# Performance work log

Hardware: AMD Instinct MI355X
Metric: run time of the kernel (lower is better)

Reference implementation:

```python
import jax, jax.numpy as jnp
import numpy as np


def squash(x, axis=-1):
    # norm_sq/(1+norm_sq) * x/norm, exactly as the torch version
    norm_sq = jnp.sum(x * x, axis=axis, keepdims=True)
    norm = jnp.sqrt(norm_sq)
    return norm_sq / (1.0 + norm_sq) * (x / norm)


def setup_inputs() -> dict:
    key = jax.random.key(0)
    k1, k2 = jax.random.split(key)
    batch, in_caps, in_hid, out_caps, out_hid = 128, 1152, 16, 32, 16
    input_capsules = jax.random.normal(k1, (batch, in_caps, in_hid), dtype=jnp.float32)
    # EinMix weight: 'in_caps in_hid out_caps out_hid'
    W = jax.random.normal(k2, (in_caps, in_hid, out_caps, out_hid), dtype=jnp.float32) * 0.05
    return {"input_capsules": input_capsules, "W": W, "routing_iterations": 3}


def reference(input_capsules, W, routing_iterations):
    # U: [batch, in_caps, out_caps, out_hid]
    U = jnp.einsum('bih,ihoj->bioj', input_capsules, W)
    batch, in_caps, out_caps, out_hid = U.shape
    B = jnp.zeros((batch, in_caps, out_caps), dtype=U.dtype)
    V = None
    for _ in range(routing_iterations):
        C = jax.nn.softmax(B, axis=-1)           # [b, i, o]
        S = jnp.einsum('bio,bioh->boh', C, U)    # [b, o, h]
        V = squash(S, axis=-1)                   # [b, o, h]
        B = B + jnp.einsum('bioh,boh->bio', U, V)
    return V
```

## Files before the change

### kernel.cpp

```cpp
#include <hip/hip_runtime.h>
#include <hip/hip_bf16.h>


#define IN_CAPS 1152
#define OUT_CAPS 32
#define BATCH 128
#define IPC 18
#define NBLK_I (IN_CAPS / IPC)
#define SV_ELEMS (BATCH * OUT_CAPS * 16)

typedef __attribute__((ext_vector_type(8))) short short8;
typedef __attribute__((ext_vector_type(4))) float f32x4;

__device__ inline unsigned f2bf(float x) {
  unsigned u = __builtin_bit_cast(unsigned, x);
  return (u + 0x7FFFu + ((u >> 16) & 1u)) >> 16;
}

__global__ __launch_bounds__(256) void conv_w(const float* __restrict__ W,
                                              unsigned short* __restrict__ Wb) {
  __shared__ float st[16 * 516];
  const int t = threadIdx.x;
  const size_t ibase = (size_t)blockIdx.x * 8192;
  const float4* src = (const float4*)(W + ibase);
#pragma unroll
  for (int r = 0; r < 8; ++r) {
    const int f = r * 256 + t;
    const int k = f >> 7, c4 = f & 127;
    *(float4*)&st[k * 516 + c4 * 4] = src[f];
  }
  __syncthreads();
  unsigned short* dst = Wb + ibase;
#pragma unroll
  for (int r = 0; r < 4; ++r) {
    const int u = r * 256 + t;
    const int o = u >> 5, l = u & 31;
    const int col = o * 16 + (l & 15), k0 = (l >> 4) * 8;
    unsigned b[8];
#pragma unroll
    for (int j = 0; j < 8; ++j) b[j] = f2bf(st[(k0 + j) * 516 + col]);
    uint4 outv;
    outv.x = b[0] | (b[1] << 16);
    outv.y = b[2] | (b[3] << 16);
    outv.z = b[4] | (b[5] << 16);
    outv.w = b[6] | (b[7] << 16);
    *(uint4*)(dst + (size_t)u * 8) = outv;
  }
}

__device__ __forceinline__ void build_xs(const float* __restrict__ X, int bg,
                                         int i0, int t, unsigned (*xs)[64][4]) {
#pragma unroll
  for (int rep = 0; rep < IPC * 256 / 512; ++rep) {
    const int base = rep * 512 + t;
    const int ii = base >> 8;
    const int e = base & 255;
    const int l2 = e >> 2, ju = e & 3;
    unsigned val = 0;
    if (l2 < 32) {
      const float2 f = *(const float2*)(X +
          ((size_t)(bg * 16 + (l2 & 15)) * IN_CAPS + (i0 + ii)) * 16 +
          (l2 >> 4) * 8 + 2 * ju);
      val = f2bf(f.x) | (f2bf(f.y) << 16);
    }
    xs[ii][l2][ju] = val;
  }
}

__device__ __forceinline__ short8 ld_x(const unsigned (*xs)[64][4], int ii, int l) {
  return __builtin_bit_cast(short8, *(const uint4*)(&xs[ii][l][0]));
}

__global__ __launch_bounds__(512, 4)
void caps_pass1(const unsigned short* __restrict__ Wb,
                const float* __restrict__ X, float* __restrict__ P) {
  __shared__ __align__(16) unsigned xs[IPC][64][4];
  const int t = threadIdx.x, w = t >> 6, l = t & 63;
  const int q = l >> 4, bl = l & 15;
  const int gx = blockIdx.x, iblk = gx & 63, bg = gx >> 6;
  const int i0 = iblk * IPC;

  build_xs(X, bg, i0, t, xs);
  __syncthreads();

  const short8* wp = (const short8*)Wb + ((size_t)i0 * 32 + w * 4) * 32 + (l & 31);
  f32x4 sacc[4];
#pragma unroll
  for (int m = 0; m < 4; ++m) sacc[m] = (f32x4){0.f, 0.f, 0.f, 0.f};

  for (int ii = 0; ii < IPC; ++ii) {
    short8 x = ld_x(xs, ii, l);
    short8 a0 = wp[0], a1 = wp[32], a2 = wp[64], a3 = wp[96];
    wp += 1024;
    sacc[0] = __builtin_amdgcn_mfma_f32_16x16x32_bf16(a0, x, sacc[0], 0, 0, 0);
    sacc[1] = __builtin_amdgcn_mfma_f32_16x16x32_bf16(a1, x, sacc[1], 0, 0, 0);
    sacc[2] = __builtin_amdgcn_mfma_f32_16x16x32_bf16(a2, x, sacc[2], 0, 0, 0);
    sacc[3] = __builtin_amdgcn_mfma_f32_16x16x32_bf16(a3, x, sacc[3], 0, 0, 0);
  }
  float* pp = P + ((size_t)iblk * 128 + bg * 16 + bl) * 512 + w * 64 + q * 4;
#pragma unroll
  for (int m = 0; m < 4; ++m) *(f32x4*)(pp + m * 16) = sacc[m] * (1.f / 32.f);
}

__global__ __launch_bounds__(512, 4)
void caps_pass23(const unsigned short* __restrict__ Wb,
                 const float* __restrict__ X,
                 const float* __restrict__ Vt,
                 float* __restrict__ P) {
  __shared__ __align__(16) unsigned xs[IPC][64][4];
  __shared__ float part[2][8][16];
  const int t = threadIdx.x, w = t >> 6, l = t & 63;
  const int q = l >> 4, bl = l & 15;
  const int gx = blockIdx.x, iblk = gx & 63, bg = gx >> 6;
  const int i0 = iblk * IPC;

  f32x4 v[4], sacc[4];
#pragma unroll
  for (int m = 0; m < 4; ++m) {
    v[m] = ((const f32x4*)Vt)[((size_t)(bg * 8 + w) * 64 + l) * 4 + m];
    sacc[m] = (f32x4){0.f, 0.f, 0.f, 0.f};
  }

  build_xs(X, bg, i0, t, xs);
  __syncthreads();

  const short8* wp = (const short8*)Wb + ((size_t)i0 * 32 + w * 4) * 32 + (l & 31);
  short8 an[4];
  short8 xn = ld_x(xs, 0, l);
#pragma unroll
  for (int m = 0; m < 4; ++m) an[m] = wp[m * 32];
  wp += 1024;

  for (int ii = 0; ii < IPC; ++ii) {
    short8 ac[4];
#pragma unroll
    for (int m = 0; m < 4; ++m) ac[m] = an[m];
    short8 xc = xn;
    if (ii + 1 < IPC) {
      xn = ld_x(xs, ii + 1, l);
#pragma unroll
      for (int m = 0; m < 4; ++m) an[m] = wp[m * 32];
      wp += 1024;
    }

    const f32x4 z = {0.f, 0.f, 0.f, 0.f};
    f32x4 d[4];
#pragma unroll
    for (int m = 0; m < 4; ++m)
      d[m] = __builtin_amdgcn_mfma_f32_16x16x32_bf16(ac[m], xc, z, 0, 0, 0);

    float e[4];
#pragma unroll
    for (int m = 0; m < 4; ++m) {
      f32x4 pr = d[m] * v[m];
      float p = (pr[0] + pr[1]) + (pr[2] + pr[3]);
      p += __shfl_xor(p, 16);
      p += __shfl_xor(p, 32);
      e[m] = __expf(p);
    }
    const float esum = (e[0] + e[1]) + (e[2] + e[3]);
    if (q == 0) part[ii & 1][w][bl] = esum;
    __syncthreads();
    float den = 0.f;
#pragma unroll
    for (int ww = 0; ww < 8; ++ww) den += part[ii & 1][ww][bl];
    const float rden = __builtin_amdgcn_rcpf(den);
#pragma unroll
    for (int m = 0; m < 4; ++m) sacc[m] += d[m] * (e[m] * rden);
  }

  float* pp = P + ((size_t)iblk * 128 + bg * 16 + bl) * 512 + w * 64 + q * 4;
#pragma unroll
  for (int m = 0; m < 4; ++m) *(f32x4*)(pp + m * 16) = sacc[m];
}

template <int MODE>
__global__ __launch_bounds__(256)
void reduce_squash(const float* __restrict__ P, float* __restrict__ Vt,
                   float* __restrict__ V1p, float* __restrict__ Out) {
  const int j = blockIdx.x * 256 + threadIdx.x;
  float s = 0.f;
  const float* p = P + j;
#pragma unroll 8
  for (int k = 0; k < NBLK_I; ++k) s += p[(size_t)k * SV_ELEMS];
  float ns = s * s;
  ns += __shfl_xor(ns, 1);
  ns += __shfl_xor(ns, 2);
  ns += __shfl_xor(ns, 4);
  ns += __shfl_xor(ns, 8);
  const float sc = ns / ((1.f + ns) * sqrtf(ns));
  float vv = s * sc;
  if constexpr (MODE == 2) {
    Out[j] = vv;
  } else {
    if constexpr (MODE == 0) V1p[j] = vv;
    if constexpr (MODE == 1) vv += V1p[j];
    const int b = j >> 9, oh = j & 511, o = oh >> 4, h = oh & 15;
    const int bg = b >> 4, bl = b & 15, w = o >> 2, m = o & 3, qq = h >> 2;
    Vt[(((size_t)(bg * 8 + w) * 64 + qq * 16 + bl) * 16) + m * 4 + (h & 3)] = vv;
  }
}

extern "C" void kernel_launch(void* const* d_in, const int* in_sizes, int n_in,
                              void* d_out, int out_size, void* d_ws, size_t ws_size,
                              hipStream_t stream) {
  const float* X  = (const float*)d_in[0];
  const float* Wg = (const float*)d_in[1];

  float* P   = (float*)d_ws;
  float* Vt  = P + (size_t)NBLK_I * SV_ELEMS;
  float* V1p = Vt + SV_ELEMS;
  unsigned short* Wb = (unsigned short*)(V1p + SV_ELEMS);
  float* out = (float*)d_out;

  conv_w<<<IN_CAPS, 256, 0, stream>>>(Wg, Wb);

  caps_pass1<<<512, 512, 0, stream>>>(Wb, X, P);
  reduce_squash<0><<<256, 256, 0, stream>>>(P, Vt, V1p, nullptr);

  caps_pass23<<<512, 512, 0, stream>>>(Wb, X, Vt, P);
  reduce_squash<1><<<256, 256, 0, stream>>>(P, Vt, V1p, nullptr);

  caps_pass23<<<512, 512, 0, stream>>>(Wb, X, Vt, P);
  reduce_squash<2><<<256, 256, 0, stream>>>(P, nullptr, nullptr, out);
}
```

Measured before the change: 164.9 us.

## Fuse all capsule routing stages into one cooperative kernel with grid syncs

Replaces the seven separate launches (weight conversion, three routing passes, three reductions) with one cooperative kernel that separates phases using grid-wide syncs. Shared memory is reused between the weight transpose staging and the X tile. The aim is to remove per-launch overhead and inter-kernel gaps. The costs are grid barrier overhead and a reduction phase that now uses only a quarter of the threads, concentrated in the first blocks. The old multi-kernel path is kept as a fallback if the cooperative launch fails.

```diff
diff --git a/kernel.cpp b/kernel.cpp
--- a/kernel.cpp
+++ b/kernel.cpp
@@ -1,5 +1,8 @@
 #include <hip/hip_runtime.h>
 #include <hip/hip_bf16.h>
+#include <hip/hip_cooperative_groups.h>
+
+namespace cg = cooperative_groups;
 
 
 #define IN_CAPS 1152
@@ -8,6 +11,7 @@
 #define IPC 18
 #define NBLK_I (IN_CAPS / IPC)
 #define SV_ELEMS (BATCH * OUT_CAPS * 16)
+#define GRID 512
 
 typedef __attribute__((ext_vector_type(8))) short short8;
 typedef __attribute__((ext_vector_type(4))) float f32x4;
@@ -15,37 +19,6 @@
 __device__ inline unsigned f2bf(float x) {
   unsigned u = __builtin_bit_cast(unsigned, x);
   return (u + 0x7FFFu + ((u >> 16) & 1u)) >> 16;
-}
-
-__global__ __launch_bounds__(256) void conv_w(const float* __restrict__ W,
-                                              unsigned short* __restrict__ Wb) {
-  __shared__ float st[16 * 516];
-  const int t = threadIdx.x;
-  const size_t ibase = (size_t)blockIdx.x * 8192;
-  const float4* src = (const float4*)(W + ibase);
-#pragma unroll
-  for (int r = 0; r < 8; ++r) {
-    const int f = r * 256 + t;
-    const int k = f >> 7, c4 = f & 127;
-    *(float4*)&st[k * 516 + c4 * 4] = src[f];
-  }
-  __syncthreads();
-  unsigned short* dst = Wb + ibase;
-#pragma unroll
-  for (int r = 0; r < 4; ++r) {
-    const int u = r * 256 + t;
-    const int o = u >> 5, l = u & 31;
-    const int col = o * 16 + (l & 15), k0 = (l >> 4) * 8;
-    unsigned b[8];
-#pragma unroll
-    for (int j = 0; j < 8; ++j) b[j] = f2bf(st[(k0 + j) * 516 + col]);
-    uint4 outv;
-    outv.x = b[0] | (b[1] << 16);
-    outv.y = b[2] | (b[3] << 16);
-    outv.z = b[4] | (b[5] << 16);
-    outv.w = b[6] | (b[7] << 16);
-    *(uint4*)(dst + (size_t)u * 8) = outv;
-  }
 }
 
 __device__ __forceinline__ void build_xs(const float* __restrict__ X, int bg,
@@ -71,23 +44,43 @@
   return __builtin_bit_cast(short8, *(const uint4*)(&xs[ii][l][0]));
 }
 
-__global__ __launch_bounds__(512, 4)
-void caps_pass1(const unsigned short* __restrict__ Wb,
-                const float* __restrict__ X, float* __restrict__ P) {
-  __shared__ __align__(16) unsigned xs[IPC][64][4];
-  const int t = threadIdx.x, w = t >> 6, l = t & 63;
-  const int q = l >> 4, bl = l & 15;
-  const int gx = blockIdx.x, iblk = gx & 63, bg = gx >> 6;
-  const int i0 = iblk * IPC;
-
-  build_xs(X, bg, i0, t, xs);
-  __syncthreads();
-
-  const short8* wp = (const short8*)Wb + ((size_t)i0 * 32 + w * 4) * 32 + (l & 31);
+__device__ __forceinline__ void conv_i(const float* __restrict__ W,
+                                       unsigned short* __restrict__ Wb,
+                                       float* st, int i, int t) {
+  const float4* src = (const float4*)(W + (size_t)i * 8192);
+#pragma unroll
+  for (int r = 0; r < 4; ++r) {
+    const int f = r * 512 + t;
+    const int k = f >> 7, c4 = f & 127;
+    *(float4*)&st[k * 516 + c4 * 4] = src[f];
+  }
+  __syncthreads();
+  unsigned short* dst = Wb + (size_t)i * 8192;
+#pragma unroll
+  for (int r = 0; r < 2; ++r) {
+    const int uu = r * 512 + t;
+    const int o = uu >> 5, ll = uu & 31;
+    const int col = o * 16 + (ll & 15), k0 = (ll >> 4) * 8;
+    unsigned b[8];
+#pragma unroll
+    for (int j = 0; j < 8; ++j) b[j] = f2bf(st[(k0 + j) * 516 + col]);
+    uint4 outv;
+    outv.x = b[0] | (b[1] << 16);
+    outv.y = b[2] | (b[3] << 16);
+    outv.z = b[4] | (b[5] << 16);
+    outv.w = b[6] | (b[7] << 16);
+    *(uint4*)(dst + (size_t)uu * 8) = outv;
+  }
+  __syncthreads();
+}
+
+__device__ __forceinline__ void pass1_phase(const short8* __restrict__ wpb,
+                                            const unsigned (*xs)[64][4],
+                                            float* __restrict__ pp, int l) {
+  const short8* wp = wpb;
   f32x4 sacc[4];
 #pragma unroll
   for (int m = 0; m < 4; ++m) sacc[m] = (f32x4){0.f, 0.f, 0.f, 0.f};
-
   for (int ii = 0; ii < IPC; ++ii) {
     short8 x = ld_x(xs, ii, l);
     short8 a0 = wp[0], a1 = wp[32], a2 = wp[64], a3 = wp[96];
@@ -97,23 +90,16 @@
     sacc[2] = __builtin_amdgcn_mfma_f32_16x16x32_bf16(a2, x, sacc[2], 0, 0, 0);
     sacc[3] = __builtin_amdgcn_mfma_f32_16x16x32_bf16(a3, x, sacc[3], 0, 0, 0);
   }
-  float* pp = P + ((size_t)iblk * 128 + bg * 16 + bl) * 512 + w * 64 + q * 4;
 #pragma unroll
   for (int m = 0; m < 4; ++m) *(f32x4*)(pp + m * 16) = sacc[m] * (1.f / 32.f);
 }
 
-__global__ __launch_bounds__(512, 4)
-void caps_pass23(const unsigned short* __restrict__ Wb,
-                 const float* __restrict__ X,
-                 const float* __restrict__ Vt,
-                 float* __restrict__ P) {
-  __shared__ __align__(16) unsigned xs[IPC][64][4];
-  __shared__ float part[2][8][16];
-  const int t = threadIdx.x, w = t >> 6, l = t & 63;
-  const int q = l >> 4, bl = l & 15;
-  const int gx = blockIdx.x, iblk = gx & 63, bg = gx >> 6;
-  const int i0 = iblk * IPC;
-
+__device__ __forceinline__ void pass23_phase(const short8* __restrict__ wpb,
+                                             const unsigned (*xs)[64][4],
+                                             float (*part)[8][16],
+                                             const float* __restrict__ Vt,
+                                             float* __restrict__ pp,
+                                             int bg, int w, int l, int q, int bl) {
   f32x4 v[4], sacc[4];
 #pragma unroll
   for (int m = 0; m < 4; ++m) {
@@ -121,10 +107,7 @@
     sacc[m] = (f32x4){0.f, 0.f, 0.f, 0.f};
   }
 
-  build_xs(X, bg, i0, t, xs);
-  __syncthreads();
-
-  const short8* wp = (const short8*)Wb + ((size_t)i0 * 32 + w * 4) * 32 + (l & 31);
+  const short8* wp = wpb;
   short8 an[4];
   short8 xn = ld_x(xs, 0, l);
 #pragma unroll
@@ -169,9 +152,139 @@
     for (int m = 0; m < 4; ++m) sacc[m] += d[m] * (e[m] * rden);
   }
 
+#pragma unroll
+  for (int m = 0; m < 4; ++m) *(f32x4*)(pp + m * 16) = sacc[m];
+}
+
+template <int MODE>
+__device__ __forceinline__ void reduce_phase(const float* __restrict__ P,
+                                             float* __restrict__ Vt,
+                                             float* __restrict__ V1p,
+                                             float* __restrict__ Out, int j) {
+  if (j < SV_ELEMS) {
+    float s = 0.f;
+    const float* p = P + j;
+#pragma unroll 8
+    for (int k = 0; k < NBLK_I; ++k) s += p[(size_t)k * SV_ELEMS];
+    float ns = s * s;
+    ns += __shfl_xor(ns, 1);
+    ns += __shfl_xor(ns, 2);
+    ns += __shfl_xor(ns, 4);
+    ns += __shfl_xor(ns, 8);
+    const float sc = ns / ((1.f + ns) * sqrtf(ns));
+    float vv = s * sc;
+    if constexpr (MODE == 2) {
+      Out[j] = vv;
+    } else {
+      if constexpr (MODE == 0) V1p[j] = vv;
+      if constexpr (MODE == 1) vv += V1p[j];
+      const int b = j >> 9, oh = j & 511, o = oh >> 4, h = oh & 15;
+      const int bg = b >> 4, bl = b & 15, w = o >> 2, m = o & 3, qq = h >> 2;
+      Vt[(((size_t)(bg * 8 + w) * 64 + qq * 16 + bl) * 16) + m * 4 + (h & 3)] = vv;
+    }
+  }
+}
+
+__global__ __launch_bounds__(512, 4)
+void caps_fused(const float* __restrict__ W, const float* __restrict__ X,
+                unsigned short* __restrict__ Wb, float* __restrict__ P,
+                float* __restrict__ Vt, float* __restrict__ V1p,
+                float* __restrict__ Out) {
+  __shared__ __align__(16) char smem[16 * 516 * 4];
+  float* st = (float*)smem;
+  unsigned (*xs)[64][4] = (unsigned (*)[64][4])smem;
+  float (*part)[8][16] = (float (*)[8][16])(smem + IPC * 64 * 16);
+
+  const int t = threadIdx.x, w = t >> 6, l = t & 63;
+  const int q = l >> 4, bl = l & 15;
+  const int bid = blockIdx.x, iblk = bid & 63, bg = bid >> 6;
+  const int i0 = iblk * IPC;
+  const int gt = bid * 512 + t;
+  cg::grid_group grid = cg::this_grid();
+
+  for (int i = bid; i < IN_CAPS; i += GRID) conv_i(W, Wb, st, i, t);
+
+  build_xs(X, bg, i0, t, xs);
+  __syncthreads();
+  grid.sync();
+
+  const short8* wpb = (const short8*)Wb + ((size_t)i0 * 32 + w * 4) * 32 + (l & 31);
   float* pp = P + ((size_t)iblk * 128 + bg * 16 + bl) * 512 + w * 64 + q * 4;
-#pragma unroll
-  for (int m = 0; m < 4; ++m) *(f32x4*)(pp + m * 16) = sacc[m];
+
+  pass1_phase(wpb, xs, pp, l);
+  grid.sync();
+  reduce_phase<0>(P, Vt, V1p, nullptr, gt);
+  grid.sync();
+  pass23_phase(wpb, xs, part, Vt, pp, bg, w, l, q, bl);
+  grid.sync();
+  reduce_phase<1>(P, Vt, V1p, nullptr, gt);
+  grid.sync();
+  pass23_phase(wpb, xs, part, Vt, pp, bg, w, l, q, bl);
+  grid.sync();
+  reduce_phase<2>(P, nullptr, nullptr, Out, gt);
+}
+
+__global__ __launch_bounds__(256) void conv_w(const float* __restrict__ W,
+                                              unsigned short* __restrict__ Wb) {
+  __shared__ float st[16 * 516];
+  const int t = threadIdx.x;
+  const size_t ibase = (size_t)blockIdx.x * 8192;
+  const float4* src = (const float4*)(W + ibase);
+#pragma unroll
+  for (int r = 0; r < 8; ++r) {
+    const int f = r * 256 + t;
+    const int k = f >> 7, c4 = f & 127;
+    *(float4*)&st[k * 516 + c4 * 4] = src[f];
+  }
+  __syncthreads();
+  unsigned short* dst = Wb + ibase;
+#pragma unroll
+  for (int r = 0; r < 4; ++r) {
+    const int u = r * 256 + t;
+    const int o = u >> 5, l = u & 31;
+    const int col = o * 16 + (l & 15), k0 = (l >> 4) * 8;
+    unsigned b[8];
+#pragma unroll
+    for (int j = 0; j < 8; ++j) b[j] = f2bf(st[(k0 + j) * 516 + col]);
+    uint4 outv;
+    outv.x = b[0] | (b[1] << 16);
+    outv.y = b[2] | (b[3] << 16);
+    outv.z = b[4] | (b[5] << 16);
+    outv.w = b[6] | (b[7] << 16);
+    *(uint4*)(dst + (size_t)u * 8) = outv;
+  }
+}
+
+__global__ __launch_bounds__(512, 4)
+void caps_pass1(const unsigned short* __restrict__ Wb,
+                const float* __restrict__ X, float* __restrict__ P) {
+  __shared__ __align__(16) unsigned xs[IPC][64][4];
+  const int t = threadIdx.x, w = t >> 6, l = t & 63;
+  const int q = l >> 4, bl = l & 15;
+  const int gx = blockIdx.x, iblk = gx & 63, bg = gx >> 6;
+  const int i0 = iblk * IPC;
+  build_xs(X, bg, i0, t, xs);
+  __syncthreads();
+  const short8* wpb = (const short8*)Wb + ((size_t)i0 * 32 + w * 4) * 32 + (l & 31);
+  float* pp = P + ((size_t)iblk * 128 + bg * 16 + bl) * 512 + w * 64 + q * 4;
+  pass1_phase(wpb, xs, pp, l);
+}
+
+__global__ __launch_bounds__(512, 4)
+void caps_pass23(const unsigned short* __restrict__ Wb,
+                 const float* __restrict__ X,
+                 const float* __restrict__ Vt, float* __restrict__ P) {
+  __shared__ __align__(16) unsigned xs[IPC][64][4];
+  __shared__ float part[2][8][16];
+  const int t = threadIdx.x, w = t >> 6, l = t & 63;
+  const int q = l >> 4, bl = l & 15;
+  const int gx = blockIdx.x, iblk = gx & 63, bg = gx >> 6;
+  const int i0 = iblk * IPC;
+  build_xs(X, bg, i0, t, xs);
+  __syncthreads();
+  const short8* wpb = (const short8*)Wb + ((size_t)i0 * 32 + w * 4) * 32 + (l & 31);
+  float* pp = P + ((size_t)iblk * 128 + bg * 16 + bl) * 512 + w * 64 + q * 4;
+  pass23_phase(wpb, xs, part, Vt, pp, bg, w, l, q, bl);
 }
 
 template <int MODE>
@@ -179,26 +292,7 @@
 void reduce_squash(const float* __restrict__ P, float* __restrict__ Vt,
                    float* __restrict__ V1p, float* __restrict__ Out) {
   const int j = blockIdx.x * 256 + threadIdx.x;
-  float s = 0.f;
-  const float* p = P + j;
-#pragma unroll 8
-  for (int k = 0; k < NBLK_I; ++k) s += p[(size_t)k * SV_ELEMS];
-  float ns = s * s;
-  ns += __shfl_xor(ns, 1);
-  ns += __shfl_xor(ns, 2);
-  ns += __shfl_xor(ns, 4);
-  ns += __shfl_xor(ns, 8);
-  const float sc = ns / ((1.f + ns) * sqrtf(ns));
-  float vv = s * sc;
-  if constexpr (MODE == 2) {
-    Out[j] = vv;
-  } else {
-    if constexpr (MODE == 0) V1p[j] = vv;
-    if constexpr (MODE == 1) vv += V1p[j];
-    const int b = j >> 9, oh = j & 511, o = oh >> 4, h = oh & 15;
-    const int bg = b >> 4, bl = b & 15, w = o >> 2, m = o & 3, qq = h >> 2;
-    Vt[(((size_t)(bg * 8 + w) * 64 + qq * 16 + bl) * 16) + m * 4 + (h & 3)] = vv;
-  }
+  reduce_phase<MODE>(P, Vt, V1p, Out, j);
 }
 
 extern "C" void kernel_launch(void* const* d_in, const int* in_sizes, int n_in,
@@ -213,14 +307,18 @@
   unsigned short* Wb = (unsigned short*)(V1p + SV_ELEMS);
   float* out = (float*)d_out;
 
-  conv_w<<<IN_CAPS, 256, 0, stream>>>(Wg, Wb);
-
-  caps_pass1<<<512, 512, 0, stream>>>(Wb, X, P);
-  reduce_squash<0><<<256, 256, 0, stream>>>(P, Vt, V1p, nullptr);
-
-  caps_pass23<<<512, 512, 0, stream>>>(Wb, X, Vt, P);
-  reduce_squash<1><<<256, 256, 0, stream>>>(P, Vt, V1p, nullptr);
-
-  caps_pass23<<<512, 512, 0, stream>>>(Wb, X, Vt, P);
-  reduce_squash<2><<<256, 256, 0, stream>>>(P, nullptr, nullptr, out);
-}
+  void* args[] = {(void*)&Wg, (void*)&X, (void*)&Wb, (void*)&P,
+                  (void*)&Vt, (void*)&V1p, (void*)&out};
+  hipError_t err = hipLaunchCooperativeKernel((void*)caps_fused, dim3(GRID),
+                                              dim3(512), args, 0, stream);
+  if (err != hipSuccess) {
+    (void)hipGetLastError();
+    conv_w<<<IN_CAPS, 256, 0, stream>>>(Wg, Wb);
+    caps_pass1<<<512, 512, 0, stream>>>(Wb, X, P);
+    reduce_squash<0><<<256, 256, 0, stream>>>(P, Vt, V1p, nullptr);
+    caps_pass23<<<512, 512, 0, stream>>>(Wb, X, Vt, P);
+    reduce_squash<1><<<256, 256, 0, stream>>>(P, Vt, V1p, nullptr);
+    caps_pass23<<<512, 512, 0, stream>>>(Wb, X, Vt, P);
+    reduce_squash<2><<<256, 256, 0, stream>>>(P, nullptr, nullptr, out);
+  }
+}
```

After: 517.8 us. 214% more time.

## Halve routing-pass barriers and parallelize partial-sum reduction across k

Applied to the files above, without the earlier changes.

The routing pass now handles two input capsules per barrier, writing softmax denominators into a four-slot shared buffer so one __syncthreads serves both. This is meant to cut barrier stalls in the latency-bound inner loop, at the cost of holding an extra set of accumulator registers. The reduce/squash kernel now uses float4 loads and splits the 64-way sum over eight thread groups, combined through shared memory, and launches twice as many blocks. This exposes more memory parallelism in the reduction but leaves only 32 threads active for the final squash.

```diff
diff --git a/kernel.cpp b/kernel.cpp
--- a/kernel.cpp
+++ b/kernel.cpp
@@ -108,7 +108,7 @@
                  const float* __restrict__ Vt,
                  float* __restrict__ P) {
   __shared__ __align__(16) unsigned xs[IPC][64][4];
-  __shared__ float part[2][8][16];
+  __shared__ float part[4][8][16];
   const int t = threadIdx.x, w = t >> 6, l = t & 63;
   const int q = l >> 4, bl = l & 15;
   const int gx = blockIdx.x, iblk = gx & 63, bg = gx >> 6;
@@ -131,42 +131,77 @@
   for (int m = 0; m < 4; ++m) an[m] = wp[m * 32];
   wp += 1024;
 
-  for (int ii = 0; ii < IPC; ++ii) {
-    short8 ac[4];
-#pragma unroll
-    for (int m = 0; m < 4; ++m) ac[m] = an[m];
-    short8 xc = xn;
-    if (ii + 1 < IPC) {
-      xn = ld_x(xs, ii + 1, l);
+  for (int pr2 = 0; pr2 < IPC / 2; ++pr2) {
+    f32x4 dk0[4], dk1[4];
+    const int s0 = (pr2 & 1) * 2;
+    {
+      short8 ac[4];
+      short8 xc = xn;
+#pragma unroll
+      for (int m = 0; m < 4; ++m) ac[m] = an[m];
+      xn = ld_x(xs, 2 * pr2 + 1, l);
 #pragma unroll
       for (int m = 0; m < 4; ++m) an[m] = wp[m * 32];
       wp += 1024;
-    }
-
-    const f32x4 z = {0.f, 0.f, 0.f, 0.f};
-    f32x4 d[4];
-#pragma unroll
-    for (int m = 0; m < 4; ++m)
-      d[m] = __builtin_amdgcn_mfma_f32_16x16x32_bf16(ac[m], xc, z, 0, 0, 0);
-
-    float e[4];
-#pragma unroll
-    for (int m = 0; m < 4; ++m) {
-      f32x4 pr = d[m] * v[m];
-      float p = (pr[0] + pr[1]) + (pr[2] + pr[3]);
-      p += __shfl_xor(p, 16);
-      p += __shfl_xor(p, 32);
-      e[m] = __expf(p);
-    }
-    const float esum = (e[0] + e[1]) + (e[2] + e[3]);
-    if (q == 0) part[ii & 1][w][bl] = esum;
+      const f32x4 z = {0.f, 0.f, 0.f, 0.f};
+      f32x4 d[4];
+      float e[4];
+#pragma unroll
+      for (int m = 0; m < 4; ++m)
+        d[m] = __builtin_amdgcn_mfma_f32_16x16x32_bf16(ac[m], xc, z, 0, 0, 0);
+#pragma unroll
+      for (int m = 0; m < 4; ++m) {
+        f32x4 pm = d[m] * v[m];
+        float p = (pm[0] + pm[1]) + (pm[2] + pm[3]);
+        p += __shfl_xor(p, 16);
+        p += __shfl_xor(p, 32);
+        e[m] = __expf(p);
+      }
+      if (q == 0) part[s0][w][bl] = (e[0] + e[1]) + (e[2] + e[3]);
+#pragma unroll
+      for (int m = 0; m < 4; ++m) dk0[m] = d[m] * e[m];
+    }
+    {
+      const int ii = 2 * pr2 + 1;
+      short8 ac[4];
+      short8 xc = xn;
+#pragma unroll
+      for (int m = 0; m < 4; ++m) ac[m] = an[m];
+      if (ii + 1 < IPC) {
+        xn = ld_x(xs, ii + 1, l);
+#pragma unroll
+        for (int m = 0; m < 4; ++m) an[m] = wp[m * 32];
+        wp += 1024;
+      }
+      const f32x4 z = {0.f, 0.f, 0.f, 0.f};
+      f32x4 d[4];
+      float e[4];
+#pragma unroll
+      for (int m = 0; m < 4; ++m)
+        d[m] = __builtin_amdgcn_mfma_f32_16x16x32_bf16(ac[m], xc, z, 0, 0, 0);
+#pragma unroll
+      for (int m = 0; m < 4; ++m) {
+        f32x4 pm = d[m] * v[m];
+        float p = (pm[0] + pm[1]) + (pm[2] + pm[3]);
+        p += __shfl_xor(p, 16);
+        p += __shfl_xor(p, 32);
+        e[m] = __expf(p);
+      }
+      if (q == 0) part[s0 + 1][w][bl] = (e[0] + e[1]) + (e[2] + e[3]);
+#pragma unroll
+      for (int m = 0; m < 4; ++m) dk1[m] = d[m] * e[m];
+    }
     __syncthreads();
-    float den = 0.f;
-#pragma unroll
-    for (int ww = 0; ww < 8; ++ww) den += part[ii & 1][ww][bl];
-    const float rden = __builtin_amdgcn_rcpf(den);
-#pragma unroll
-    for (int m = 0; m < 4; ++m) sacc[m] += d[m] * (e[m] * rden);
+    float den0 = 0.f, den1 = 0.f;
+#pragma unroll
+    for (int ww = 0; ww < 8; ++ww) {
+      den0 += part[s0][ww][bl];
+      den1 += part[s0 + 1][ww][bl];
+    }
+    const float r0 = __builtin_amdgcn_rcpf(den0);
+    const float r1 = __builtin_amdgcn_rcpf(den1);
+#pragma unroll
+    for (int m = 0; m < 4; ++m) sacc[m] += dk0[m] * r0 + dk1[m] * r1;
   }
 
   float* pp = P + ((size_t)iblk * 128 + bg * 16 + bl) * 512 + w * 64 + q * 4;
@@ -178,26 +213,38 @@
 __global__ __launch_bounds__(256)
 void reduce_squash(const float* __restrict__ P, float* __restrict__ Vt,
                    float* __restrict__ V1p, float* __restrict__ Out) {
-  const int j = blockIdx.x * 256 + threadIdx.x;
-  float s = 0.f;
-  const float* p = P + j;
-#pragma unroll 8
-  for (int k = 0; k < NBLK_I; ++k) s += p[(size_t)k * SV_ELEMS];
-  float ns = s * s;
-  ns += __shfl_xor(ns, 1);
-  ns += __shfl_xor(ns, 2);
-  ns += __shfl_xor(ns, 4);
-  ns += __shfl_xor(ns, 8);
-  const float sc = ns / ((1.f + ns) * sqrtf(ns));
-  float vv = s * sc;
-  if constexpr (MODE == 2) {
-    Out[j] = vv;
-  } else {
-    if constexpr (MODE == 0) V1p[j] = vv;
-    if constexpr (MODE == 1) vv += V1p[j];
-    const int b = j >> 9, oh = j & 511, o = oh >> 4, h = oh & 15;
-    const int bg = b >> 4, bl = b & 15, w = o >> 2, m = o & 3, qq = h >> 2;
-    Vt[(((size_t)(bg * 8 + w) * 64 + qq * 16 + bl) * 16) + m * 4 + (h & 3)] = vv;
+  __shared__ f32x4 red[8][32];
+  const int t = threadIdx.x, qd = t & 31, kq = t >> 5;
+  const int j4 = blockIdx.x * 32 + qd;
+  const f32x4* p = (const f32x4*)P + j4 + (size_t)kq * 8 * (SV_ELEMS / 4);
+  f32x4 s = {0.f, 0.f, 0.f, 0.f};
+#pragma unroll
+  for (int k = 0; k < 8; ++k) s += p[(size_t)k * (SV_ELEMS / 4)];
+  red[kq][qd] = s;
+  __syncthreads();
+  if (t < 32) {
+    f32x4 a = red[0][t];
+#pragma unroll
+    for (int k2 = 1; k2 < 8; ++k2) a += red[k2][t];
+    float ns = a[0] * a[0] + a[1] * a[1] + a[2] * a[2] + a[3] * a[3];
+    ns += __shfl_xor(ns, 1);
+    ns += __shfl_xor(ns, 2);
+    const float sc = ns / ((1.f + ns) * sqrtf(ns));
+    f32x4 vv = a * sc;
+    if constexpr (MODE == 2) {
+      ((f32x4*)Out)[j4] = vv;
+    } else {
+      if constexpr (MODE == 0) ((f32x4*)V1p)[j4] = vv;
+      if constexpr (MODE == 1) vv += ((const f32x4*)V1p)[j4];
+#pragma unroll
+      for (int c = 0; c < 4; ++c) {
+        const int j = j4 * 4 + c;
+        const int b = j >> 9, oh = j & 511, o = oh >> 4, h = oh & 15;
+        const int bg = b >> 4, bl = b & 15, w = o >> 2, m = o & 3, qq = h >> 2;
+        Vt[(((size_t)(bg * 8 + w) * 64 + qq * 16 + bl) * 16) + m * 4 + (h & 3)] =
+            vv[c];
+      }
+    }
   }
 }
 
@@ -216,11 +263,11 @@
   conv_w<<<IN_CAPS, 256, 0, stream>>>(Wg, Wb);
 
   caps_pass1<<<512, 512, 0, stream>>>(Wb, X, P);
-  reduce_squash<0><<<256, 256, 0, stream>>>(P, Vt, V1p, nullptr);
+  reduce_squash<0><<<512, 256, 0, stream>>>(P, Vt, V1p, nullptr);
 
   caps_pass23<<<512, 512, 0, stream>>>(Wb, X, Vt, P);
-  reduce_squash<1><<<256, 256, 0, stream>>>(P, Vt, V1p, nullptr);
+  reduce_squash<1><<<512, 256, 0, stream>>>(P, Vt, V1p, nullptr);
 
   caps_pass23<<<512, 512, 0, stream>>>(Wb, X, Vt, P);
-  reduce_squash<2><<<256, 256, 0, stream>>>(P, nullptr, nullptr, out);
-}
+  reduce_squash<2><<<512, 256, 0, stream>>>(P, nullptr, nullptr, out);
+}
```

Result: faster. 161.4 us (-2.1%).
